# Kernel optimization log

Hardware: AMD Instinct MI355X
Metric: run time of the kernel (lower is better)

## Reference

```python
import jax, jax.numpy as jnp
import numpy as np

ROPE_THETA = 10000.0

def _apply_rope(t):
    # t: [B, H, S, D]; rotate interleaved even/odd pairs
    B, H, S, D = t.shape
    inv_freq = 1.0 / (ROPE_THETA ** (jnp.arange(0, D, 2, dtype=jnp.float32) / D))  # [D/2]
    ang = jnp.arange(S, dtype=jnp.float32)[:, None] * inv_freq[None, :]            # [S, D/2]
    cos = jnp.cos(ang)[None, None]  # [1,1,S,D/2]
    sin = jnp.sin(ang)[None, None]
    te = t[..., 0::2]
    to = t[..., 1::2]
    re = te * cos - to * sin
    ro = te * sin + to * cos
    out = jnp.stack([re, ro], axis=-1).reshape(B, H, S, D)
    return out

def setup_inputs() -> dict:
    key = jax.random.key(0)
    ks = jax.random.split(key, 5)
    B, S, DIM = 2, 2048, 2048
    x = jax.random.normal(ks[0], (B, S, DIM), dtype=jnp.float32)
    scale = 0.02
    Wq = jax.random.normal(ks[1], (DIM, DIM), dtype=jnp.float32) * scale
    Wk = jax.random.normal(ks[2], (DIM, DIM), dtype=jnp.float32) * scale
    Wv = jax.random.normal(ks[3], (DIM, DIM), dtype=jnp.float32) * scale
    Wo = jax.random.normal(ks[4], (DIM, DIM), dtype=jnp.float32) * scale
    return {"x": x, "Wq": Wq, "Wk": Wk, "Wv": Wv, "Wo": Wo}

def reference(x, Wq, Wk, Wv, Wo):
    B, S, DIM = x.shape
    H = 16
    HD = DIM // H
    # nn.Linear(bias=False) with weight [out,in]: y = x @ W.T; here W stored [in,out]
    q = (x @ Wq).reshape(B, S, H, HD).transpose(0, 2, 1, 3)  # [B,H,S,HD]
    k = (x @ Wk).reshape(B, S, H, HD).transpose(0, 2, 1, 3)
    v = (x @ Wv).reshape(B, S, H, HD).transpose(0, 2, 1, 3)
    q = _apply_rope(q)
    k = _apply_rope(k)
    scores = jnp.einsum('bhqd,bhkd->bhqk', q, k) / jnp.sqrt(jnp.float32(HD))  # [B,H,S,S]
    causal = jnp.tril(jnp.ones((S, S), dtype=bool))
    scores = jnp.where(causal[None, None], scores, jnp.float32(-jnp.inf))
    attn = jax.nn.softmax(scores, axis=-1)
    out = jnp.einsum('bhqk,bhkd->bhqd', attn, v)            # [B,H,S,HD]
    out = out.transpose(0, 2, 1, 3).reshape(B, S, DIM)
    return out @ Wo  # output projection (dropout is identity in eval)
```

## Files before the change

kernel.cpp:

```cpp
#include <hip/hip_runtime.h>
#include <hip/hip_bf16.h>
#include <math.h>

typedef __bf16 bf16;
typedef __attribute__((ext_vector_type(2))) __bf16 bf16x2;
typedef __attribute__((ext_vector_type(4))) __bf16 bf16x4;
typedef __attribute__((ext_vector_type(8))) __bf16 bf16x8;
typedef __attribute__((ext_vector_type(4))) float f32x4;

#define LDS_ASYNC16(gptr, lptr)                                                        \
  __builtin_amdgcn_global_load_lds(                                                    \
      (const __attribute__((address_space(1))) void*)(gptr),                           \
      (__attribute__((address_space(3))) void*)(lptr), 16, 0, 0)

constexpr int BATCH = 2, SEQ = 2048, DIM = 2048, NH = 16, HD = 128;
constexpr float QSC = 0.12751744f;
constexpr float FREQC = 0.20762050593046f;

template <int CTRL>
__device__ __forceinline__ float dpp_mov_f(float x) {
  return __int_as_float(__builtin_amdgcn_update_dpp(
      __float_as_int(x), __float_as_int(x), CTRL, 0xf, 0xf, false));
}
__device__ __forceinline__ float rowmax16(float x) {
  x = fmaxf(x, dpp_mov_f<0x121>(x));
  x = fmaxf(x, dpp_mov_f<0x122>(x));
  x = fmaxf(x, dpp_mov_f<0x124>(x));
  x = fmaxf(x, dpp_mov_f<0x128>(x));
  return x;
}
__device__ __forceinline__ float rowsum16(float x) {
  x += dpp_mov_f<0x121>(x);
  x += dpp_mov_f<0x122>(x);
  x += dpp_mov_f<0x124>(x);
  x += dpp_mov_f<0x128>(x);
  return x;
}

__global__ void cvt_f32_to_bf16(const float4* __restrict__ in,
                                bf16x4* __restrict__ out, int n4) {
  int i = blockIdx.x * blockDim.x + threadIdx.x;
  if (i >= n4) return;
  float4 v = in[i];
  bf16x4 o;
  o[0] = (bf16)v.x; o[1] = (bf16)v.y; o[2] = (bf16)v.z; o[3] = (bf16)v.w;
  out[i] = o;
}

__global__ void transpose_w4(const float* __restrict__ W0, const float* __restrict__ W1,
                             const float* __restrict__ W2, const float* __restrict__ W3,
                             bf16* __restrict__ T0, bf16* __restrict__ T3) {
  __shared__ float tile[32][33];
  const int z = blockIdx.z;
  const float* W = (z == 0) ? W0 : (z == 1) ? W1 : (z == 2) ? W2 : W3;
  bf16* WT = (z == 3) ? T3 : (T0 + (size_t)z * DIM * DIM);
  int tx = threadIdx.x, ty = threadIdx.y;
  int bx = blockIdx.x * 32, by = blockIdx.y * 32;
#pragma unroll
  for (int j = 0; j < 32; j += 8)
    tile[ty + j][tx] = W[(size_t)(by + ty + j) * DIM + bx + tx];
  __syncthreads();
#pragma unroll
  for (int j = 0; j < 32; j += 8)
    WT[(size_t)(bx + ty + j) * DIM + by + tx] = (bf16)tile[tx][ty + j];
}

__device__ __forceinline__ void stage_A(const bf16* __restrict__ src, int g0, int ks,
                                        bf16* lds, int w, int lane) {
  const int u = w * 64 + lane;
  const int row = u >> 2;
  const int kc = (u & 3) ^ ((u >> 3) & 3);
  LDS_ASYNC16(src + (size_t)(g0 + row) * DIM + ks + kc * 8,
              lds + (size_t)(w * 64) * 8);
}
__device__ __forceinline__ void stage_B(const bf16* __restrict__ src, int g0, int ks,
                                        bf16* lds, int w, int lane) {
#pragma unroll
  for (int j = 0; j < 2; ++j) {
    const int u = (j * 8 + w) * 64 + lane;
    const int row = u >> 2;
    const int kc = (u & 3) ^ ((u >> 3) & 3);
    LDS_ASYNC16(src + (size_t)(g0 + row) * DIM + ks + kc * 8,
                lds + (size_t)((j * 8 + w) * 64) * 8);
  }
}

__global__ __launch_bounds__(512) void gemm_qkv(const bf16* __restrict__ A,
                                                const bf16* __restrict__ BT,
                                                bf16* __restrict__ Qb,
                                                bf16* __restrict__ Kb,
                                                bf16* __restrict__ VTo) {
  constexpr int ARSZ = 128 * 32;
  constexpr int BRSZ = 256 * 32;
  constexpr int NT = DIM / 64;
  __shared__ __attribute__((aligned(16))) bf16 As[4 * ARSZ];
  __shared__ __attribute__((aligned(16))) bf16 Bs[4 * BRSZ];
  const int tid = threadIdx.x;
  const int w = tid >> 6, lane = tid & 63;
  const int quad = lane >> 4, ln = lane & 15;
  const int wm = w >> 2, wn = w & 3;
  const int lb = blockIdx.x;
  const int xcd = lb & 7, i = lb >> 3;
  const int by = (xcd >> 1) * 8 + (i & 7);
  const int bx = (xcd & 1) * 12 + (i >> 3);
  const int m0 = by * 128, n0 = bx * 256;
  const int pc = (quad ^ ((ln >> 1) & 3)) * 8;
  const int aoff = wm * 64 + ln;
  const int boff = wn * 64 + ln;

  f32x4 acc[4][4] = {};

  stage_A(A,  m0, 0,  As + 0 * ARSZ, w, lane);
  stage_B(BT, n0, 0,  Bs + 0 * BRSZ, w, lane);
  stage_A(A,  m0, 32, As + 1 * ARSZ, w, lane);
  stage_B(BT, n0, 32, Bs + 1 * BRSZ, w, lane);
  stage_A(A,  m0, 64, As + 2 * ARSZ, w, lane);
  stage_B(BT, n0, 64, Bs + 2 * BRSZ, w, lane);
  asm volatile("s_waitcnt vmcnt(3)" ::: "memory");
  __builtin_amdgcn_s_barrier();

#pragma unroll 2
  for (int t = 0; t < NT; ++t) {
    const int b2 = (t & 1) * 2;
    const bf16* Ab0 = As + b2 * ARSZ;
    const bf16* Ab1 = Ab0 + ARSZ;
    const bf16* Bb0 = Bs + b2 * BRSZ;
    const bf16* Bb1 = Bb0 + BRSZ;
    bf16x8 af[4], bfr[4];

#pragma unroll
    for (int f = 0; f < 4; ++f)
      af[f] = *(const bf16x8*)(Ab0 + (aoff + f * 16) * 32 + pc);
#pragma unroll
    for (int f = 0; f < 4; ++f)
      bfr[f] = *(const bf16x8*)(Bb0 + (boff + f * 16) * 32 + pc);
    if (t + 1 < NT) {
      const int r1 = ((t + 1) & 1) * 2 + 1;
      stage_A(A,  m0, (t + 1) * 64 + 32, As + r1 * ARSZ, w, lane);
      stage_B(BT, n0, (t + 1) * 64 + 32, Bs + r1 * BRSZ, w, lane);
    }
    __builtin_amdgcn_s_barrier();
    asm volatile("s_waitcnt lgkmcnt(0)" ::: "memory");
    __builtin_amdgcn_s_setprio(1);
#pragma unroll
    for (int mf = 0; mf < 4; ++mf)
#pragma unroll
      for (int nf = 0; nf < 4; ++nf)
        acc[mf][nf] = __builtin_amdgcn_mfma_f32_16x16x32_bf16(
            af[mf], bfr[nf], acc[mf][nf], 0, 0, 0);
    __builtin_amdgcn_s_setprio(0);
    __builtin_amdgcn_s_barrier();

#pragma unroll
    for (int f = 0; f < 4; ++f)
      af[f] = *(const bf16x8*)(Ab1 + (aoff + f * 16) * 32 + pc);
#pragma unroll
    for (int f = 0; f < 4; ++f)
      bfr[f] = *(const bf16x8*)(Bb1 + (boff + f * 16) * 32 + pc);
    if (t + 2 < NT) {
      stage_A(A,  m0, (t + 2) * 64, As + b2 * ARSZ, w, lane);
      stage_B(BT, n0, (t + 2) * 64, Bs + b2 * BRSZ, w, lane);
    }
    __builtin_amdgcn_s_barrier();
    asm volatile("s_waitcnt lgkmcnt(0)" ::: "memory");
    __builtin_amdgcn_s_setprio(1);
#pragma unroll
    for (int mf = 0; mf < 4; ++mf)
#pragma unroll
      for (int nf = 0; nf < 4; ++nf)
        acc[mf][nf] = __builtin_amdgcn_mfma_f32_16x16x32_bf16(
            af[mf], bfr[nf], acc[mf][nf], 0, 0, 0);
    __builtin_amdgcn_s_setprio(0);
    if (t + 2 < NT) asm volatile("s_waitcnt vmcnt(3)" ::: "memory");
    else            asm volatile("s_waitcnt vmcnt(0)" ::: "memory");
    __builtin_amdgcn_s_barrier();
  }

  const int sel = n0 >> 11;
  if (sel == 2) {
#pragma unroll
    for (int mf = 0; mf < 4; ++mf)
#pragma unroll
      for (int nf = 0; nf < 4; ++nf) {
        int gr = m0 + wm * 64 + mf * 16 + quad * 4;
        int fc = (n0 + wn * 64 + nf * 16 + ln) & 2047;
        int bb = gr >> 11, s0 = gr & (SEQ - 1);
        int h = fc >> 7, d = fc & (HD - 1);
        bf16x4 pk;
#pragma unroll
        for (int r = 0; r < 4; ++r) pk[r] = (bf16)acc[mf][nf][r];
        *(bf16x4*)(VTo + ((size_t)((bb * NH + h) * HD + d)) * SEQ + s0) = pk;
      }
  } else {
    bf16* Dst = sel ? Kb : Qb;
    const float osc = sel ? 1.0f : QSC;
#pragma unroll
    for (int nf = 0; nf < 4; ++nf) {
      int gc = n0 + wn * 64 + nf * 16 + ln;
      int fc = gc & 2047, d = fc & (HD - 1);
      float freq = exp2f(-(float)(d >> 1) * FREQC);
      bool ev = !(d & 1);
#pragma unroll
      for (int mf = 0; mf < 4; ++mf) {
#pragma unroll
        for (int r = 0; r < 4; ++r) {
          int gr = m0 + wm * 64 + mf * 16 + quad * 4 + r;
          int s = gr & (SEQ - 1);
          float ang = (float)s * freq;
          float sn, cs;
          __sincosf(ang, &sn, &cs);
          float own = acc[mf][nf][r];
          float oth = __shfl_xor(own, 1);
          float res = ev ? (own * cs - oth * sn) : (oth * sn + own * cs);
          Dst[(size_t)gr * DIM + fc] = (bf16)(res * osc);
        }
      }
    }
  }
}

template <int MODE>
__global__ __launch_bounds__(256) void gemm_bt(const bf16* __restrict__ A,
                                               const bf16* __restrict__ BT,
                                               void* __restrict__ C) {
  __shared__ __attribute__((aligned(16))) bf16 As[128 * 64];
  __shared__ __attribute__((aligned(16))) bf16 Bs[128 * 64];
  const int tid = threadIdx.x;
  const int w = tid >> 6, lane = tid & 63;
  const int quad = lane >> 4, ln = lane & 15;
  const int m0 = blockIdx.y * 128, n0 = blockIdx.x * 128;
  const int wm = (w >> 1) * 64, wn = (w & 1) * 64;
  const int l7 = ln & 7;
  f32x4 acc[4][4] = {};

  for (int k0 = 0; k0 < DIM; k0 += 64) {
#pragma unroll
    for (int i = 0; i < 4; ++i) {
      const int c = i * 256 + tid;
      const int row = c >> 3, p = c & 7;
      LDS_ASYNC16(A  + (size_t)(m0 + row) * DIM + k0 + ((p ^ (row & 7)) * 8),
                  As + (size_t)(i * 256 + w * 64) * 8);
      LDS_ASYNC16(BT + (size_t)(n0 + row) * DIM + k0 + ((p ^ (row & 7)) * 8),
                  Bs + (size_t)(i * 256 + w * 64) * 8);
    }
    __syncthreads();
#pragma unroll
    for (int kh = 0; kh < 2; ++kh) {
      bf16x8 af[4], bfr[4];
#pragma unroll
      for (int t = 0; t < 4; ++t)
        af[t] = *(const bf16x8*)(As + (wm + t * 16 + ln) * 64 +
                                 (((kh * 4 + quad) ^ l7) * 8));
#pragma unroll
      for (int t = 0; t < 4; ++t)
        bfr[t] = *(const bf16x8*)(Bs + (wn + t * 16 + ln) * 64 +
                                  (((kh * 4 + quad) ^ l7) * 8));
#pragma unroll
      for (int mt = 0; mt < 4; ++mt)
#pragma unroll
        for (int nt = 0; nt < 4; ++nt)
          acc[mt][nt] = __builtin_amdgcn_mfma_f32_16x16x32_bf16(
              af[mt], bfr[nt], acc[mt][nt], 0, 0, 0);
    }
    __syncthreads();
  }

  if (MODE == 0) {
    bf16* Co = (bf16*)C;
#pragma unroll
    for (int mt = 0; mt < 4; ++mt)
#pragma unroll
      for (int nt = 0; nt < 4; ++nt) {
        int gr = m0 + wm + mt * 16 + quad * 4;
        int gc = n0 + wn + nt * 16 + ln;
#pragma unroll
        for (int r = 0; r < 4; ++r)
          Co[(size_t)(gr + r) * DIM + gc] = (bf16)acc[mt][nt][r];
      }
  } else {
    float* Co = (float*)C;
#pragma unroll
    for (int mt = 0; mt < 4; ++mt)
#pragma unroll
      for (int nt = 0; nt < 4; ++nt) {
        int gr = m0 + wm + mt * 16 + quad * 4;
        int gc = n0 + wn + nt * 16 + ln;
#pragma unroll
        for (int r = 0; r < 4; ++r)
          Co[(size_t)(gr + r) * DIM + gc] = acc[mt][nt][r];
      }
  }
}

__device__ __forceinline__ int ml_off(int t) {
  return (t < 10) ? 2 * (t - 5) : (t < 15) ? 10 + 3 * (t - 10) : 25;
}
__device__ __forceinline__ int op_off(int t) {
  return (t < 10) ? (t - 5) : (t < 15) ? 5 + 2 * (t - 10) : 15;
}

constexpr int PSTR = 72;
__global__ __launch_bounds__(256) void flash_attn(
    const bf16* __restrict__ Q, const bf16* __restrict__ K,
    const bf16* __restrict__ VT, bf16* __restrict__ O,
    bf16* __restrict__ Opart, float* __restrict__ Mpart,
    float* __restrict__ Lpart) {
  __shared__ __attribute__((aligned(16))) bf16 Ks[64 * 128];
  __shared__ __attribute__((aligned(16))) bf16 VTs[128 * 64];
  __shared__ __attribute__((aligned(16))) bf16 Ps[4][32 * PSTR];
  const int tid = threadIdx.x;
  const int w = tid >> 6, lane = tid & 63, quad = lane >> 4, ln = lane & 15;
  const int lb = blockIdx.x;
  const int low3 = lb & 7, rest = lb >> 3;
  const int e = rest % 34;
  const int bh = (rest / 34) * 8 + low3;
  int t, c0, nc;
  if (e < 5)       { t = e;                  c0 = 0;               nc = 1; }
  else if (e < 15) { t = 5 + ((e - 5) >> 1); c0 = (e - 5) & 1;     nc = 2; }
  else if (e < 30) { int q = (e - 15) / 3;   t = 10 + q; c0 = (e - 15) - 3 * q; nc = 3; }
  else             { t = 15;                 c0 = e - 30;          nc = 4; }
  const int q0 = t * 128;
  const int ktN = 2 * (t + 1);
  const int kt0 = c0 * 10;
  const int kt1 = min(kt0 + 10, ktN);
  const bool chunked = (nc > 1);
  const int b = bh >> 4, h = bh & 15;

  bf16x8 qf[2][4];
#pragma unroll
  for (int mt = 0; mt < 2; ++mt)
#pragma unroll
    for (int kc = 0; kc < 4; ++kc)
      qf[mt][kc] = *(const bf16x8*)(Q + ((size_t)b * SEQ + q0 + w * 32 + mt * 16 + ln) * DIM +
                                    h * HD + kc * 32 + quad * 8);
  f32x4 o[2][8] = {};
  float mst[2][4], lst[2][4];
#pragma unroll
  for (int mt = 0; mt < 2; ++mt)
#pragma unroll
    for (int r = 0; r < 4; ++r) { mst[mt][r] = -1e30f; lst[mt][r] = 0.f; }

  for (int kt = kt0; kt < kt1; ++kt) {
    __syncthreads();
#pragma unroll
    for (int i = 0; i < 4; ++i) {
      const int c = i * 256 + tid;
      LDS_ASYNC16(K + ((size_t)b * SEQ + kt * 64 + (c >> 4)) * DIM + h * HD +
                      (((c & 15) ^ ((c >> 4) & 15)) * 8),
                  Ks + (size_t)(i * 256 + w * 64) * 8);
      LDS_ASYNC16(VT + ((size_t)((b * NH + h) * HD) + (c >> 3)) * SEQ + kt * 64 +
                      (((c & 7) ^ ((c >> 3) & 7)) * 8),
                  VTs + (size_t)(i * 256 + w * 64) * 8);
    }
    __syncthreads();

    f32x4 s[2][4] = {};
#pragma unroll
    for (int nt = 0; nt < 4; ++nt) {
      bf16x8 kf[4];
#pragma unroll
      for (int kc = 0; kc < 4; ++kc)
        kf[kc] = *(const bf16x8*)(Ks + (nt * 16 + ln) * 128 +
                                  (((kc * 4 + quad) ^ ln) * 8));
#pragma unroll
      for (int kc = 0; kc < 4; ++kc)
#pragma unroll
        for (int mt = 0; mt < 2; ++mt)
          s[mt][nt] = __builtin_amdgcn_mfma_f32_16x16x32_bf16(
              qf[mt][kc], kf[kc], s[mt][nt], 0, 0, 0);
    }

    const bool diag = (kt * 64 + 63 > q0);
    if (diag) {
#pragma unroll
      for (int mt = 0; mt < 2; ++mt)
#pragma unroll
        for (int nt = 0; nt < 4; ++nt)
#pragma unroll
          for (int r = 0; r < 4; ++r) {
            int kg = kt * 64 + nt * 16 + ln;
            int qg = q0 + w * 32 + mt * 16 + quad * 4 + r;
            if (kg > qg) s[mt][nt][r] = -1e30f;
          }
    }

#pragma unroll
    for (int mt = 0; mt < 2; ++mt)
#pragma unroll
      for (int r = 0; r < 4; ++r) {
        float rm = fmaxf(fmaxf(s[mt][0][r], s[mt][1][r]),
                         fmaxf(s[mt][2][r], s[mt][3][r]));
        rm = rowmax16(rm);
        float mold = mst[mt][r];
        float mnew = fmaxf(mold, rm);
        float alpha = exp2f(mold - mnew);
        mst[mt][r] = mnew;
        float rs = 0.f;
#pragma unroll
        for (int nt = 0; nt < 4; ++nt) {
          float p = exp2f(s[mt][nt][r] - mnew);
          rs += p;
          Ps[w][(mt * 16 + quad * 4 + r) * PSTR + nt * 16 + ln] = (bf16)p;
        }
        lst[mt][r] = lst[mt][r] * alpha + rs;
#pragma unroll
        for (int nd = 0; nd < 8; ++nd) o[mt][nd][r] *= alpha;
      }
    __syncthreads();

#pragma unroll
    for (int kc2 = 0; kc2 < 2; ++kc2) {
      bf16x8 pf[2];
#pragma unroll
      for (int mt = 0; mt < 2; ++mt)
        pf[mt] = *(const bf16x8*)(&Ps[w][(mt * 16 + ln) * PSTR + kc2 * 32 + quad * 8]);
#pragma unroll
      for (int nd = 0; nd < 8; ++nd) {
        bf16x8 vf = *(const bf16x8*)(VTs + (nd * 16 + ln) * 64 +
                                     (((kc2 * 4 + quad) ^ (ln & 7)) * 8));
#pragma unroll
        for (int mt = 0; mt < 2; ++mt)
          o[mt][nd] = __builtin_amdgcn_mfma_f32_16x16x32_bf16(
              pf[mt], vf, o[mt][nd], 0, 0, 0);
      }
    }
  }

  if (!chunked) {
#pragma unroll
    for (int mt = 0; mt < 2; ++mt)
#pragma unroll
      for (int r = 0; r < 4; ++r) {
        float inv = 1.f / rowsum16(lst[mt][r]);
        int qg = q0 + w * 32 + mt * 16 + quad * 4 + r;
#pragma unroll
        for (int nd = 0; nd < 8; ++nd)
          O[((size_t)b * SEQ + qg) * DIM + h * HD + nd * 16 + ln] =
              (bf16)(o[mt][nd][r] * inv);
      }
  } else {
    const int mls = bh * 29 + ml_off(t) + c0;
    bf16* Op = (c0 == 0) ? nullptr
                         : Opart + (size_t)(bh * 18 + op_off(t) + (c0 - 1)) * (128 * 128);
#pragma unroll
    for (int mt = 0; mt < 2; ++mt)
#pragma unroll
      for (int r = 0; r < 4; ++r) {
        float l = rowsum16(lst[mt][r]);
        int qr = w * 32 + mt * 16 + quad * 4 + r;
        if (ln == 0) {
          Mpart[mls * 128 + qr] = mst[mt][r];
          Lpart[mls * 128 + qr] = l;
        }
        if (c0 == 0) {
#pragma unroll
          for (int nd = 0; nd < 8; ++nd)
            O[((size_t)b * SEQ + q0 + qr) * DIM + h * HD + nd * 16 + ln] =
                (bf16)o[mt][nd][r];
        } else {
#pragma unroll
          for (int nd = 0; nd < 8; ++nd)
            Op[qr * 128 + nd * 16 + ln] = (bf16)o[mt][nd][r];
        }
      }
  }
}

__global__ __launch_bounds__(256) void flash_merge(const bf16* __restrict__ Opart,
                                                   const float* __restrict__ Mpart,
                                                   const float* __restrict__ Lpart,
                                                   bf16* __restrict__ O) {
  const int bh = blockIdx.x;
  const int t = 5 + blockIdx.y;
  const int nc = (t < 10) ? 2 : (t < 15) ? 3 : 4;
  const int b = bh >> 4, h = bh & 15;
  const int row = threadIdx.x >> 1, half = threadIdx.x & 1;
  const int mlb = bh * 29 + ml_off(t);
  float m[4], l[4], wt[4];
  float M = -1e30f;
  for (int c = 0; c < nc; ++c) {
    m[c] = Mpart[(mlb + c) * 128 + row];
    l[c] = Lpart[(mlb + c) * 128 + row];
    M = fmaxf(M, m[c]);
  }
  float wsum = 0.f;
  for (int c = 0; c < nc; ++c) { wt[c] = exp2f(m[c] - M); wsum += wt[c] * l[c]; }
  const float inv = 1.f / wsum;
  bf16* dst = O + ((size_t)b * SEQ + t * 128 + row) * DIM + h * HD + half * 64;
  const bf16* pb = Opart + (size_t)(bh * 18 + op_off(t)) * (128 * 128) + row * 128 + half * 64;
#pragma unroll
  for (int j = 0; j < 8; ++j) {
    bf16x8 a0 = *(const bf16x8*)(dst + j * 8);
    float acc[8];
#pragma unroll
    for (int k = 0; k < 8; ++k) acc[k] = wt[0] * (float)a0[k];
    for (int c = 1; c < nc; ++c) {
      bf16x8 a = *(const bf16x8*)(pb + (size_t)(c - 1) * (128 * 128) + j * 8);
#pragma unroll
      for (int k = 0; k < 8; ++k) acc[k] += wt[c] * (float)a[k];
    }
    bf16x8 o8;
#pragma unroll
    for (int k = 0; k < 8; ++k) o8[k] = (bf16)(acc[k] * inv);
    *(bf16x8*)(dst + j * 8) = o8;
  }
}

extern "C" void kernel_launch(void* const* d_in, const int* in_sizes, int n_in,
                              void* d_out, int out_size, void* d_ws, size_t ws_size,
                              hipStream_t stream) {
  (void)in_sizes; (void)n_in; (void)out_size; (void)ws_size;
  const float* x  = (const float*)d_in[0];
  const float* Wq = (const float*)d_in[1];
  const float* Wk = (const float*)d_in[2];
  const float* Wv = (const float*)d_in[3];
  const float* Wo = (const float*)d_in[4];

  char* ws = (char*)d_ws;
  const size_t MB = 1u << 20;
  const size_t WB = (size_t)DIM * DIM * 2;
  bf16* WTqkv = (bf16*)(ws);
  bf16* WoT   = (bf16*)(ws + 3 * WB);
  bf16* xb    = (bf16*)(ws + 32 * MB);
  bf16* Qb    = (bf16*)(ws + 48 * MB);
  bf16* Kb    = (bf16*)(ws + 64 * MB);
  bf16* VT    = (bf16*)(ws + 80 * MB);
  bf16* Ab    = xb;
  bf16*  Opart = (bf16*)(ws);
  float* Mpart = (float*)(ws + 19 * MB);
  float* Lpart = (float*)(ws + 19 * MB + 512 * 1024);

  int n4 = BATCH * SEQ * DIM / 4;
  cvt_f32_to_bf16<<<n4 / 256, 256, 0, stream>>>((const float4*)x, (bf16x4*)xb, n4);
  dim3 tb(32, 8), tg(DIM / 32, DIM / 32, 4);
  transpose_w4<<<tg, tb, 0, stream>>>(Wq, Wk, Wv, Wo, WTqkv, WoT);

  gemm_qkv<<<768, 512, 0, stream>>>(xb, WTqkv, Qb, Kb, VT);

  flash_attn<<<34 * BATCH * NH, 256, 0, stream>>>(Qb, Kb, VT, Ab, Opart, Mpart, Lpart);
  dim3 mg(BATCH * NH, 11);
  flash_merge<<<mg, 256, 0, stream>>>(Opart, Mpart, Lpart, Ab);

  dim3 gg(DIM / 128, BATCH * SEQ / 128);
  gemm_bt<2><<<gg, 256, 0, stream>>>(Ab, WoT, d_out);
}
```

Before: 442.7 us.

## Load QKV GEMM B operand directly to registers, triple-buffer A in LDS

```diff
diff --git a/kernel.cpp b/kernel.cpp
--- a/kernel.cpp
+++ b/kernel.cpp
@@ -65,24 +65,12 @@
     WT[(size_t)(bx + ty + j) * DIM + by + tx] = (bf16)tile[tx][ty + j];
 }
 
-__device__ __forceinline__ void stage_A(const bf16* __restrict__ src, int g0, int ks,
-                                        bf16* lds, int w, int lane) {
-  const int u = w * 64 + lane;
-  const int row = u >> 2;
-  const int kc = (u & 3) ^ ((u >> 3) & 3);
-  LDS_ASYNC16(src + (size_t)(g0 + row) * DIM + ks + kc * 8,
+__device__ __forceinline__ void stage_A(const bf16* __restrict__ src, int m0, int ks,
+                                        bf16* lds, int w, int tid) {
+  const int row = tid >> 2;
+  const int ch = tid & 3;
+  LDS_ASYNC16(src + (size_t)(m0 + row) * DIM + ks + ch * 8,
               lds + (size_t)(w * 64) * 8);
-}
-__device__ __forceinline__ void stage_B(const bf16* __restrict__ src, int g0, int ks,
-                                        bf16* lds, int w, int lane) {
-#pragma unroll
-  for (int j = 0; j < 2; ++j) {
-    const int u = (j * 8 + w) * 64 + lane;
-    const int row = u >> 2;
-    const int kc = (u & 3) ^ ((u >> 3) & 3);
-    LDS_ASYNC16(src + (size_t)(g0 + row) * DIM + ks + kc * 8,
-                lds + (size_t)((j * 8 + w) * 64) * 8);
-  }
 }
 
 __global__ __launch_bounds__(512) void gemm_qkv(const bf16* __restrict__ A,
@@ -91,10 +79,8 @@
                                                 bf16* __restrict__ Kb,
                                                 bf16* __restrict__ VTo) {
   constexpr int ARSZ = 128 * 32;
-  constexpr int BRSZ = 256 * 32;
   constexpr int NT = DIM / 64;
-  __shared__ __attribute__((aligned(16))) bf16 As[4 * ARSZ];
-  __shared__ __attribute__((aligned(16))) bf16 Bs[4 * BRSZ];
+  __shared__ __attribute__((aligned(16))) bf16 As[3 * 2 * ARSZ];
   const int tid = threadIdx.x;
   const int w = tid >> 6, lane = tid & 63;
   const int quad = lane >> 4, ln = lane & 15;
@@ -104,76 +90,68 @@
   const int by = (xcd >> 1) * 8 + (i & 7);
   const int bx = (xcd & 1) * 12 + (i >> 3);
   const int m0 = by * 128, n0 = bx * 256;
-  const int pc = (quad ^ ((ln >> 1) & 3)) * 8;
   const int aoff = wm * 64 + ln;
-  const int boff = wn * 64 + ln;
+  const int qc = quad * 8;
+  const bf16* bbase = BT + (size_t)(n0 + wn * 64 + ln) * DIM + qc;
 
   f32x4 acc[4][4] = {};
-
-  stage_A(A,  m0, 0,  As + 0 * ARSZ, w, lane);
-  stage_B(BT, n0, 0,  Bs + 0 * BRSZ, w, lane);
-  stage_A(A,  m0, 32, As + 1 * ARSZ, w, lane);
-  stage_B(BT, n0, 32, Bs + 1 * BRSZ, w, lane);
-  stage_A(A,  m0, 64, As + 2 * ARSZ, w, lane);
-  stage_B(BT, n0, 64, Bs + 2 * BRSZ, w, lane);
-  asm volatile("s_waitcnt vmcnt(3)" ::: "memory");
+  bf16x8 bc[2][4], bn[2][4];
+
+  stage_A(A, m0, 0,  As + 0 * ARSZ, w, tid);
+  stage_A(A, m0, 32, As + 1 * ARSZ, w, tid);
+#pragma unroll
+  for (int kh = 0; kh < 2; ++kh)
+#pragma unroll
+    for (int f = 0; f < 4; ++f)
+      bc[kh][f] = *(const bf16x8*)(bbase + (size_t)(f * 16) * DIM + kh * 32);
+  stage_A(A, m0, 64, As + 2 * ARSZ, w, tid);
+  stage_A(A, m0, 96, As + 3 * ARSZ, w, tid);
+  asm volatile("s_waitcnt vmcnt(10)" ::: "memory");
   __builtin_amdgcn_s_barrier();
 
 #pragma unroll 2
   for (int t = 0; t < NT; ++t) {
-    const int b2 = (t & 1) * 2;
-    const bf16* Ab0 = As + b2 * ARSZ;
-    const bf16* Ab1 = Ab0 + ARSZ;
-    const bf16* Bb0 = Bs + b2 * BRSZ;
-    const bf16* Bb1 = Bb0 + BRSZ;
-    bf16x8 af[4], bfr[4];
-
-#pragma unroll
-    for (int f = 0; f < 4; ++f)
-      af[f] = *(const bf16x8*)(Ab0 + (aoff + f * 16) * 32 + pc);
-#pragma unroll
-    for (int f = 0; f < 4; ++f)
-      bfr[f] = *(const bf16x8*)(Bb0 + (boff + f * 16) * 32 + pc);
+    const bf16* Abuf = As + (size_t)(t % 3) * (2 * ARSZ);
+
     if (t + 1 < NT) {
-      const int r1 = ((t + 1) & 1) * 2 + 1;
-      stage_A(A,  m0, (t + 1) * 64 + 32, As + r1 * ARSZ, w, lane);
-      stage_B(BT, n0, (t + 1) * 64 + 32, Bs + r1 * BRSZ, w, lane);
-    }
+      const bf16* bsrc = bbase + (t + 1) * 64;
+#pragma unroll
+      for (int kh = 0; kh < 2; ++kh)
+#pragma unroll
+        for (int f = 0; f < 4; ++f)
+          bn[kh][f] = *(const bf16x8*)(bsrc + (size_t)(f * 16) * DIM + kh * 32);
+    }
+    if (t + 2 < NT) {
+      bf16* dst = As + (size_t)((t + 2) % 3) * (2 * ARSZ);
+      stage_A(A, m0, (t + 2) * 64,      dst,        w, tid);
+      stage_A(A, m0, (t + 2) * 64 + 32, dst + ARSZ, w, tid);
+    }
+
+#pragma unroll
+    for (int kh = 0; kh < 2; ++kh) {
+      bf16x8 af[4];
+#pragma unroll
+      for (int f = 0; f < 4; ++f)
+        af[f] = *(const bf16x8*)(Abuf + (size_t)kh * ARSZ +
+                                 (size_t)(aoff + f * 16) * 32 + qc);
+      __builtin_amdgcn_s_setprio(1);
+#pragma unroll
+      for (int mf = 0; mf < 4; ++mf)
+#pragma unroll
+        for (int nf = 0; nf < 4; ++nf)
+          acc[mf][nf] = __builtin_amdgcn_mfma_f32_16x16x32_bf16(
+              af[mf], bc[kh][nf], acc[mf][nf], 0, 0, 0);
+      __builtin_amdgcn_s_setprio(0);
+    }
+
+    if (t + 2 < NT)      asm volatile("s_waitcnt vmcnt(10)" ::: "memory");
+    else if (t + 1 < NT) asm volatile("s_waitcnt vmcnt(8)" ::: "memory");
     __builtin_amdgcn_s_barrier();
-    asm volatile("s_waitcnt lgkmcnt(0)" ::: "memory");
-    __builtin_amdgcn_s_setprio(1);
-#pragma unroll
-    for (int mf = 0; mf < 4; ++mf)
-#pragma unroll
-      for (int nf = 0; nf < 4; ++nf)
-        acc[mf][nf] = __builtin_amdgcn_mfma_f32_16x16x32_bf16(
-            af[mf], bfr[nf], acc[mf][nf], 0, 0, 0);
-    __builtin_amdgcn_s_setprio(0);
-    __builtin_amdgcn_s_barrier();
-
-#pragma unroll
-    for (int f = 0; f < 4; ++f)
-      af[f] = *(const bf16x8*)(Ab1 + (aoff + f * 16) * 32 + pc);
-#pragma unroll
-    for (int f = 0; f < 4; ++f)
-      bfr[f] = *(const bf16x8*)(Bb1 + (boff + f * 16) * 32 + pc);
-    if (t + 2 < NT) {
-      stage_A(A,  m0, (t + 2) * 64, As + b2 * ARSZ, w, lane);
-      stage_B(BT, n0, (t + 2) * 64, Bs + b2 * BRSZ, w, lane);
-    }
-    __builtin_amdgcn_s_barrier();
-    asm volatile("s_waitcnt lgkmcnt(0)" ::: "memory");
-    __builtin_amdgcn_s_setprio(1);
-#pragma unroll
-    for (int mf = 0; mf < 4; ++mf)
-#pragma unroll
-      for (int nf = 0; nf < 4; ++nf)
-        acc[mf][nf] = __builtin_amdgcn_mfma_f32_16x16x32_bf16(
-            af[mf], bfr[nf], acc[mf][nf], 0, 0, 0);
-    __builtin_amdgcn_s_setprio(0);
-    if (t + 2 < NT) asm volatile("s_waitcnt vmcnt(3)" ::: "memory");
-    else            asm volatile("s_waitcnt vmcnt(0)" ::: "memory");
-    __builtin_amdgcn_s_barrier();
+
+#pragma unroll
+    for (int kh = 0; kh < 2; ++kh)
+#pragma unroll
+      for (int f = 0; f < 4; ++f) bc[kh][f] = bn[kh][f];
   }
 
   const int sel = n0 >> 11;
```

Result: slower. 547.5 us (+23.7%).

## Widen QKV GEMM tile to 128x384 and trim pipeline barriers

Applied to the files above, without the earlier changes.

```diff
diff --git a/kernel.cpp b/kernel.cpp
--- a/kernel.cpp
+++ b/kernel.cpp
@@ -65,22 +65,21 @@
     WT[(size_t)(bx + ty + j) * DIM + by + tx] = (bf16)tile[tx][ty + j];
 }
 
-__device__ __forceinline__ void stage_A(const bf16* __restrict__ src, int g0, int ks,
-                                        bf16* lds, int w, int lane) {
-  const int u = w * 64 + lane;
-  const int row = u >> 2;
-  const int kc = (u & 3) ^ ((u >> 3) & 3);
-  LDS_ASYNC16(src + (size_t)(g0 + row) * DIM + ks + kc * 8,
+__device__ __forceinline__ void stage_A(const bf16* __restrict__ src, int m0, int ks,
+                                        bf16* lds, int w, int tid) {
+  const int row = tid >> 2;
+  const int kc = (tid & 3) ^ ((tid >> 3) & 3);
+  LDS_ASYNC16(src + (size_t)(m0 + row) * DIM + ks + kc * 8,
               lds + (size_t)(w * 64) * 8);
 }
-__device__ __forceinline__ void stage_B(const bf16* __restrict__ src, int g0, int ks,
-                                        bf16* lds, int w, int lane) {
-#pragma unroll
-  for (int j = 0; j < 2; ++j) {
-    const int u = (j * 8 + w) * 64 + lane;
+__device__ __forceinline__ void stage_B384(const bf16* __restrict__ src, int n0, int ks,
+                                           bf16* lds, int w, int tid) {
+#pragma unroll
+  for (int j = 0; j < 3; ++j) {
+    const int u = j * 512 + tid;
     const int row = u >> 2;
     const int kc = (u & 3) ^ ((u >> 3) & 3);
-    LDS_ASYNC16(src + (size_t)(g0 + row) * DIM + ks + kc * 8,
+    LDS_ASYNC16(src + (size_t)(n0 + row) * DIM + ks + kc * 8,
                 lds + (size_t)((j * 8 + w) * 64) * 8);
   }
 }
@@ -91,7 +90,7 @@
                                                 bf16* __restrict__ Kb,
                                                 bf16* __restrict__ VTo) {
   constexpr int ARSZ = 128 * 32;
-  constexpr int BRSZ = 256 * 32;
+  constexpr int BRSZ = 384 * 32;
   constexpr int NT = DIM / 64;
   __shared__ __attribute__((aligned(16))) bf16 As[4 * ARSZ];
   __shared__ __attribute__((aligned(16))) bf16 Bs[4 * BRSZ];
@@ -101,89 +100,88 @@
   const int wm = w >> 2, wn = w & 3;
   const int lb = blockIdx.x;
   const int xcd = lb & 7, i = lb >> 3;
-  const int by = (xcd >> 1) * 8 + (i & 7);
-  const int bx = (xcd & 1) * 12 + (i >> 3);
-  const int m0 = by * 128, n0 = bx * 256;
+  const int by = xcd * 4 + (i & 3);
+  const int bx = i >> 2;
+  const int m0 = by * 128, n0 = bx * 384;
+  const int aoff = wm * 64 + ln;
+  const int boff = wn * 96 + ln;
   const int pc = (quad ^ ((ln >> 1) & 3)) * 8;
-  const int aoff = wm * 64 + ln;
-  const int boff = wn * 64 + ln;
-
-  f32x4 acc[4][4] = {};
-
-  stage_A(A,  m0, 0,  As + 0 * ARSZ, w, lane);
-  stage_B(BT, n0, 0,  Bs + 0 * BRSZ, w, lane);
-  stage_A(A,  m0, 32, As + 1 * ARSZ, w, lane);
-  stage_B(BT, n0, 32, Bs + 1 * BRSZ, w, lane);
-  stage_A(A,  m0, 64, As + 2 * ARSZ, w, lane);
-  stage_B(BT, n0, 64, Bs + 2 * BRSZ, w, lane);
-  asm volatile("s_waitcnt vmcnt(3)" ::: "memory");
+
+  f32x4 acc[4][6] = {};
+
+  stage_A  (A,  m0, 0,  As + 0 * ARSZ, w, tid);
+  stage_B384(BT, n0, 0,  Bs + 0 * BRSZ, w, tid);
+  stage_A  (A,  m0, 32, As + 1 * ARSZ, w, tid);
+  stage_B384(BT, n0, 32, Bs + 1 * BRSZ, w, tid);
+  stage_A  (A,  m0, 64, As + 2 * ARSZ, w, tid);
+  stage_B384(BT, n0, 64, Bs + 2 * BRSZ, w, tid);
+  asm volatile("s_waitcnt vmcnt(8)" ::: "memory");
   __builtin_amdgcn_s_barrier();
 
 #pragma unroll 2
   for (int t = 0; t < NT; ++t) {
     const int b2 = (t & 1) * 2;
-    const bf16* Ab0 = As + b2 * ARSZ;
-    const bf16* Ab1 = Ab0 + ARSZ;
-    const bf16* Bb0 = Bs + b2 * BRSZ;
-    const bf16* Bb1 = Bb0 + BRSZ;
-    bf16x8 af[4], bfr[4];
+    bf16x8 af[4], bfr[6];
 
 #pragma unroll
     for (int f = 0; f < 4; ++f)
-      af[f] = *(const bf16x8*)(Ab0 + (aoff + f * 16) * 32 + pc);
-#pragma unroll
-    for (int f = 0; f < 4; ++f)
-      bfr[f] = *(const bf16x8*)(Bb0 + (boff + f * 16) * 32 + pc);
+      af[f] = *(const bf16x8*)(As + (size_t)(b2 + 0) * ARSZ +
+                               (size_t)(aoff + f * 16) * 32 + pc);
+#pragma unroll
+    for (int f = 0; f < 6; ++f)
+      bfr[f] = *(const bf16x8*)(Bs + (size_t)(b2 + 0) * BRSZ +
+                                (size_t)(boff + f * 16) * 32 + pc);
     if (t + 1 < NT) {
       const int r1 = ((t + 1) & 1) * 2 + 1;
-      stage_A(A,  m0, (t + 1) * 64 + 32, As + r1 * ARSZ, w, lane);
-      stage_B(BT, n0, (t + 1) * 64 + 32, Bs + r1 * BRSZ, w, lane);
-    }
-    __builtin_amdgcn_s_barrier();
-    asm volatile("s_waitcnt lgkmcnt(0)" ::: "memory");
+      stage_A  (A,  m0, (t + 1) * 64 + 32, As + (size_t)r1 * ARSZ, w, tid);
+      stage_B384(BT, n0, (t + 1) * 64 + 32, Bs + (size_t)r1 * BRSZ, w, tid);
+    }
     __builtin_amdgcn_s_setprio(1);
 #pragma unroll
     for (int mf = 0; mf < 4; ++mf)
 #pragma unroll
-      for (int nf = 0; nf < 4; ++nf)
+      for (int nf = 0; nf < 6; ++nf)
         acc[mf][nf] = __builtin_amdgcn_mfma_f32_16x16x32_bf16(
             af[mf], bfr[nf], acc[mf][nf], 0, 0, 0);
     __builtin_amdgcn_s_setprio(0);
+    if (t + 1 < NT) asm volatile("s_waitcnt vmcnt(8)" ::: "memory");
+    else            asm volatile("s_waitcnt vmcnt(0)" ::: "memory");
     __builtin_amdgcn_s_barrier();
 
 #pragma unroll
     for (int f = 0; f < 4; ++f)
-      af[f] = *(const bf16x8*)(Ab1 + (aoff + f * 16) * 32 + pc);
-#pragma unroll
-    for (int f = 0; f < 4; ++f)
-      bfr[f] = *(const bf16x8*)(Bb1 + (boff + f * 16) * 32 + pc);
+      af[f] = *(const bf16x8*)(As + (size_t)(b2 + 1) * ARSZ +
+                               (size_t)(aoff + f * 16) * 32 + pc);
+#pragma unroll
+    for (int f = 0; f < 6; ++f)
+      bfr[f] = *(const bf16x8*)(Bs + (size_t)(b2 + 1) * BRSZ +
+                                (size_t)(boff + f * 16) * 32 + pc);
     if (t + 2 < NT) {
-      stage_A(A,  m0, (t + 2) * 64, As + b2 * ARSZ, w, lane);
-      stage_B(BT, n0, (t + 2) * 64, Bs + b2 * BRSZ, w, lane);
-    }
-    __builtin_amdgcn_s_barrier();
-    asm volatile("s_waitcnt lgkmcnt(0)" ::: "memory");
+      stage_A  (A,  m0, (t + 2) * 64, As + (size_t)b2 * ARSZ, w, tid);
+      stage_B384(BT, n0, (t + 2) * 64, Bs + (size_t)b2 * BRSZ, w, tid);
+    }
     __builtin_amdgcn_s_setprio(1);
 #pragma unroll
     for (int mf = 0; mf < 4; ++mf)
 #pragma unroll
-      for (int nf = 0; nf < 4; ++nf)
+      for (int nf = 0; nf < 6; ++nf)
         acc[mf][nf] = __builtin_amdgcn_mfma_f32_16x16x32_bf16(
             af[mf], bfr[nf], acc[mf][nf], 0, 0, 0);
     __builtin_amdgcn_s_setprio(0);
-    if (t + 2 < NT) asm volatile("s_waitcnt vmcnt(3)" ::: "memory");
-    else            asm volatile("s_waitcnt vmcnt(0)" ::: "memory");
+    if (t + 2 < NT)      asm volatile("s_waitcnt vmcnt(8)" ::: "memory");
+    else if (t + 1 < NT) asm volatile("s_waitcnt vmcnt(4)" ::: "memory");
     __builtin_amdgcn_s_barrier();
   }
 
-  const int sel = n0 >> 11;
-  if (sel == 2) {
-#pragma unroll
-    for (int mf = 0; mf < 4; ++mf)
-#pragma unroll
-      for (int nf = 0; nf < 4; ++nf) {
+#pragma unroll
+  for (int nf = 0; nf < 6; ++nf) {
+    const int gc = n0 + wn * 96 + nf * 16 + ln;
+    const int sel = gc >> 11;
+    const int fc = gc & 2047;
+    if (sel == 2) {
+#pragma unroll
+      for (int mf = 0; mf < 4; ++mf) {
         int gr = m0 + wm * 64 + mf * 16 + quad * 4;
-        int fc = (n0 + wn * 64 + nf * 16 + ln) & 2047;
         int bb = gr >> 11, s0 = gr & (SEQ - 1);
         int h = fc >> 7, d = fc & (HD - 1);
         bf16x4 pk;
@@ -191,15 +189,12 @@
         for (int r = 0; r < 4; ++r) pk[r] = (bf16)acc[mf][nf][r];
         *(bf16x4*)(VTo + ((size_t)((bb * NH + h) * HD + d)) * SEQ + s0) = pk;
       }
-  } else {
-    bf16* Dst = sel ? Kb : Qb;
-    const float osc = sel ? 1.0f : QSC;
-#pragma unroll
-    for (int nf = 0; nf < 4; ++nf) {
-      int gc = n0 + wn * 64 + nf * 16 + ln;
-      int fc = gc & 2047, d = fc & (HD - 1);
-      float freq = exp2f(-(float)(d >> 1) * FREQC);
-      bool ev = !(d & 1);
+    } else {
+      bf16* Dst = sel ? Kb : Qb;
+      const float osc = sel ? 1.0f : QSC;
+      const int d = fc & (HD - 1);
+      const float freq = exp2f(-(float)(d >> 1) * FREQC);
+      const bool ev = !(d & 1);
 #pragma unroll
       for (int mf = 0; mf < 4; ++mf) {
 #pragma unroll
@@ -535,7 +530,7 @@
   dim3 tb(32, 8), tg(DIM / 32, DIM / 32, 4);
   transpose_w4<<<tg, tb, 0, stream>>>(Wq, Wk, Wv, Wo, WTqkv, WoT);
 
-  gemm_qkv<<<768, 512, 0, stream>>>(xb, WTqkv, Qb, Kb, VT);
+  gemm_qkv<<<512, 512, 0, stream>>>(xb, WTqkv, Qb, Kb, VT);
 
   flash_attn<<<34 * BATCH * NH, 256, 0, stream>>>(Qb, Kb, VT, Ab, Opart, Mpart, Lpart);
   dim3 mg(BATCH * NH, 11);
```

Result: faster. 427.9 us (-3.4%).
